# Kernel optimization log

Measured on AMD Instinct MI355X. Metric: run time of the kernel, lower is better.

Reference implementation:

```python
import jax, jax.numpy as jnp
import numpy as np

C = 256          # hidden_size
H = 8            # num_heads
HD = C // H      # head dim = 32
W = 8            # window side; N = W*W = 64 tokens per window
N = W * W
NW = 64          # windows per image
B = 32           # images
B_ = B * NW      # 2048


def make_rel_index():
    # identical to the torch buffer construction (meshgrid 'ij')
    coords = np.stack(np.meshgrid(np.arange(W), np.arange(W), indexing='ij'))  # (2,W,W)
    flat = coords.reshape(2, -1)                       # (2, N)
    rel = flat[:, :, None] - flat[:, None, :]          # (2, N, N)
    rel = rel.transpose(1, 2, 0).astype(np.int64)      # (N, N, 2)
    rel[..., 0] += W - 1
    rel[..., 1] += W - 1
    rel[..., 0] *= 2 * W - 1
    return jnp.asarray(rel.sum(-1), jnp.int32)         # (N, N) in [0, 225)


def setup_inputs() -> dict:
    key = jax.random.key(0)
    ks = jax.random.split(key, 12)
    x = jax.random.normal(ks[0], (B_, N, C), jnp.float32)
    # Swin-style additive mask: 0 for allowed, -1e9 for masked pairs
    keep = jax.random.uniform(ks[1], (NW, N, N)) > 0.1
    mask = jnp.where(keep, 0.0, -1e9).astype(jnp.float32)
    std = 0.02
    wq = jax.random.normal(ks[2], (C, C), jnp.float32) * std
    bq = jnp.zeros((C,), jnp.float32)
    wk = jax.random.normal(ks[3], (C, C), jnp.float32) * std
    bk = jnp.zeros((C,), jnp.float32)
    wv = jax.random.normal(ks[4], (C, C), jnp.float32) * std
    bv = jnp.zeros((C,), jnp.float32)
    wp = jax.random.normal(ks[5], (C, C), jnp.float32) * std
    bp = jnp.zeros((C,), jnp.float32)
    bias_table = jax.random.normal(ks[6], ((2 * W - 1) ** 2, H), jnp.float32) * std
    rel_index = make_rel_index()
    return {"x": x, "mask": mask, "wq": wq, "bq": bq, "wk": wk, "bk": bk,
            "wv": wv, "bv": bv, "wp": wp, "bp": bp,
            "bias_table": bias_table, "rel_index": rel_index}


def reference(x, mask, wq, bq, wk, bk, wv, bv, wp, bp, bias_table, rel_index):
    B_, N, C = x.shape
    nW = mask.shape[0]
    H = bias_table.shape[1]
    HD = C // H
    scale = HD ** -0.5

    def heads(t):  # (B_, N, C) -> (B_, H, N, HD)
        return t.reshape(B_, N, H, HD).transpose(0, 2, 1, 3)

    q = heads(x @ wq + bq) * scale
    k = heads(x @ wk + bk)
    v = heads(x @ wv + bv)

    attn = jnp.einsum('bhnd,bhmd->bhnm', q, k)            # (B_, H, N, N)
    bias = bias_table[rel_index]                          # (N, N, H)
    attn = attn + bias.transpose(2, 0, 1)[None]           # + (1, H, N, N)
    # add per-window shift mask, broadcast over batch and heads
    attn = attn.reshape(B_ // nW, nW, H, N, N) + mask[None, :, None]
    attn = jax.nn.softmax(attn.reshape(B_, H, N, N), axis=-1)

    out = jnp.einsum('bhnm,bhmd->bhnd', attn, v)          # (B_, H, N, HD)
    out = out.transpose(0, 2, 1, 3).reshape(B_, N, C)
    return out @ wp + bp
```

## Files before the change

### kernel.cpp

```cpp
#include <hip/hip_runtime.h>
#include <hip/hip_bf16.h>

typedef __bf16 bf16;
typedef __bf16 bf16x4 __attribute__((ext_vector_type(4)));
typedef __bf16 bf16x8 __attribute__((ext_vector_type(8)));
typedef float  f32x4  __attribute__((ext_vector_type(4)));
typedef short  s16x4  __attribute__((ext_vector_type(4)));

#define DEVI __device__ __forceinline__

static constexpr float kScale = 0.17677669529663687f;

DEVI f32x4 mfma32(bf16x8 a, bf16x8 b, f32x4 c) {
  return __builtin_amdgcn_mfma_f32_16x16x32_bf16(a, b, c, 0, 0, 0);
}
DEVI f32x4 mfma16(bf16x4 a, bf16x4 b, f32x4 c) {
#if __has_builtin(__builtin_amdgcn_mfma_f32_16x16x16bf16_1k)
  return __builtin_amdgcn_mfma_f32_16x16x16bf16_1k(
      __builtin_bit_cast(s16x4, a), __builtin_bit_cast(s16x4, b), c, 0, 0, 0);
#else
  f32x4 d;
  asm volatile("v_mfma_f32_16x16x16_bf16 %0, %1, %2, %3"
               : "=v"(d)
               : "v"(a), "v"(b), "v"(c));
  return d;
#endif
}
DEVI bf16x4 pk4(f32x4 v) {
  bf16x4 p;
  p[0] = (bf16)v[0]; p[1] = (bf16)v[1]; p[2] = (bf16)v[2]; p[3] = (bf16)v[3];
  return p;
}

__global__ __launch_bounds__(256) void prep_kernel(
    const float* __restrict__ wq, const float* __restrict__ bq,
    const float* __restrict__ wk, const float* __restrict__ bk,
    const float* __restrict__ wv, const float* __restrict__ bv,
    const float* __restrict__ wp,
    const float* __restrict__ bias_table, const int* __restrict__ rel_index,
    const float* __restrict__ mask,
    char* __restrict__ wstream, char* __restrict__ wpstream,
    float* __restrict__ bqkv, float* __restrict__ biasM) {
  int idx = blockIdx.x * 256 + threadIdx.x;
  if (idx < 196608) {
    int m = idx >> 16, n = idx & 255, k = (idx >> 8) & 255;
    const float* w = (m == 0) ? wq : (m == 1 ? wk : wv);
    float v = w[k * 256 + n];
    if (m == 0) v *= kScale;
    *(bf16*)(wstream + (size_t)(m * 8 + (k >> 5)) * 16384 + n * 64 +
             (((k & 31) * 2) ^ ((n & 3) << 4))) = (bf16)v;
  } else if (idx < 262144) {
    int rem = idx - 196608;
    int n = rem & 255, k = (rem >> 8) & 255;
    *(bf16*)(wpstream + (size_t)(k >> 5) * 16384 + n * 64 +
             (((k & 31) * 2) ^ ((n & 3) << 4))) = (bf16)wp[k * 256 + n];
  } else if (idx < 262912) {
    int rem = idx - 262144;
    int m = rem >> 8, n = rem & 255;
    const float* b = (m == 0) ? bq : (m == 1 ? bk : bv);
    float v = b[n];
    if (m == 0) v *= kScale;
    bqkv[rem] = v;
  } else if (idx < 2360064) {
    int rem = idx - 262912;
    int w = rem >> 15, h = (rem >> 12) & 7, ij = rem & 4095;
    biasM[rem] = bias_table[rel_index[ij] * 8 + h] + mask[w * 4096 + ij];
  }
}

__global__ __launch_bounds__(256, 2) void swin_kernel(
    const float* __restrict__ x, const char* __restrict__ wstream,
    const char* __restrict__ wpstream, const float* __restrict__ bqkv,
    const float* __restrict__ bp, const float* __restrict__ biasM,
    float* __restrict__ out) {
  __shared__ __align__(16) char xs_ob[32768];
  __shared__ __align__(16) char wbuf[32768];

  int tid = threadIdx.x;
  int w = tid >> 6, lane = tid & 63;
  int g = lane >> 4, c = lane & 15;
  int bid = blockIdx.x;
  int win = (bid & 7) * 256 + ((bid >> 3) & 3) * 64 + (bid >> 5);
  const f32x4 fz = {0.f, 0.f, 0.f, 0.f};

  {
    const char* xw = (const char*)(x + (size_t)win * 16384);
#pragma unroll
    for (int i = 0; i < 8; ++i) {
      int gb = i * 8192 + tid * 32;
      float4 f0 = *(const float4*)(xw + gb);
      float4 f1 = *(const float4*)(xw + gb + 16);
      bf16x8 v;
      v[0] = (bf16)f0.x; v[1] = (bf16)f0.y; v[2] = (bf16)f0.z; v[3] = (bf16)f0.w;
      v[4] = (bf16)f1.x; v[5] = (bf16)f1.y; v[6] = (bf16)f1.z; v[7] = (bf16)f1.w;
      int t = gb >> 10, ir = (gb & 1023) >> 1;
      *(bf16x8*)(xs_ob + ((t * 512 + ir) ^ ((t & 7) << 4))) = v;
    }
  }
  bf16x8 gr[4];
#pragma unroll
  for (int j = 0; j < 4; ++j)
    gr[j] = *(const bf16x8*)(wstream + (size_t)j * 4096 + (size_t)tid * 16);
#pragma unroll
  for (int j = 0; j < 4; ++j)
    *(bf16x8*)(wbuf + j * 4096 + tid * 16) = gr[j];
#pragma unroll
  for (int j = 0; j < 4; ++j)
    gr[j] = *(const bf16x8*)(wstream + 16384 + (size_t)j * 4096 + (size_t)tid * 16);
  __syncthreads();

  bf16x4 qp[4][4], kp[4][4], vp[4][4];
  f32x4 acc[4][4];

  for (int i = 0; i < 24; ++i) {
    int m = i >> 3, kq = i & 7;
    char* cur = wbuf + (i & 1) * 16384;
    char* nxt = wbuf + ((i + 1) & 1) * 16384;

    bf16x8 xf[4], wf[4];
#pragma unroll
    for (int tt = 0; tt < 4; ++tt)
      xf[tt] = *(const bf16x8*)(
          xs_ob + (((tt * 16 + c) * 512 + kq * 64 + g * 16) ^ ((c & 7) << 4)));
#pragma unroll
    for (int nt = 0; nt < 4; ++nt)
      wf[nt] = *(const bf16x8*)(
          cur + (w * 64 + nt * 16 + c) * 64 + ((g * 16) ^ ((c & 3) << 4)));

#pragma unroll
    for (int j = 0; j < 4; ++j)
      *(bf16x8*)(nxt + j * 4096 + tid * 16) = gr[j];
    {
      const char* src = (i < 22) ? (wstream + (size_t)(i + 2) * 16384)
                                 : (wpstream + (size_t)(i - 22) * 16384);
#pragma unroll
      for (int j = 0; j < 4; ++j)
        gr[j] = *(const bf16x8*)(src + (size_t)j * 4096 + (size_t)tid * 16);
    }

    if (kq == 0) {
      if (m < 2) {
#pragma unroll
        for (int nt = 0; nt < 4; ++nt) {
          f32x4 b4 = *(const f32x4*)(bqkv + m * 256 + w * 64 + nt * 16 + g * 4);
#pragma unroll
          for (int tt = 0; tt < 4; ++tt) acc[tt][nt] = b4;
        }
      } else {
#pragma unroll
        for (int nt = 0; nt < 4; ++nt) {
          float bv_ = bqkv[512 + w * 64 + nt * 16 + c];
          f32x4 b4 = {bv_, bv_, bv_, bv_};
#pragma unroll
          for (int tt = 0; tt < 4; ++tt) acc[tt][nt] = b4;
        }
      }
    }
    if (m < 2) {
#pragma unroll
      for (int tt = 0; tt < 4; ++tt)
#pragma unroll
        for (int nt = 0; nt < 4; ++nt)
          acc[tt][nt] = mfma32(wf[nt], xf[tt], acc[tt][nt]);
    } else {
#pragma unroll
      for (int tt = 0; tt < 4; ++tt)
#pragma unroll
        for (int nt = 0; nt < 4; ++nt)
          acc[tt][nt] = mfma32(xf[tt], wf[nt], acc[tt][nt]);
    }
    if (kq == 7) {
#pragma unroll
      for (int tt = 0; tt < 4; ++tt)
#pragma unroll
        for (int nt = 0; nt < 4; ++nt) {
          if (m == 0)      qp[tt][nt] = pk4(acc[tt][nt]);
          else if (m == 1) kp[tt][nt] = pk4(acc[tt][nt]);
          else             vp[tt][nt] = pk4(acc[tt][nt]);
        }
    }
    __syncthreads();
  }

#pragma unroll
  for (int hh = 0; hh < 2; ++hh) {
    int h = w * 2 + hh;
    const float* bm = biasM + ((size_t)(win & 63) * 8 + h) * 4096;
#pragma unroll
    for (int mi = 0; mi < 4; ++mi) {
      f32x4 s[4];
#pragma unroll
      for (int mj = 0; mj < 4; ++mj)
        s[mj] = *(const f32x4*)(bm + (mi * 16 + c) * 64 + mj * 16 + g * 4);
#pragma unroll
      for (int dd = 0; dd < 2; ++dd)
#pragma unroll
        for (int mj = 0; mj < 4; ++mj)
          s[mj] = mfma16(kp[mj][hh * 2 + dd], qp[mi][hh * 2 + dd], s[mj]);
      float mx;
      {
        f32x4 m4 = s[0];
#pragma unroll
        for (int mj = 1; mj < 4; ++mj) {
          m4[0] = fmaxf(m4[0], s[mj][0]); m4[1] = fmaxf(m4[1], s[mj][1]);
          m4[2] = fmaxf(m4[2], s[mj][2]); m4[3] = fmaxf(m4[3], s[mj][3]);
        }
        mx = fmaxf(fmaxf(m4[0], m4[1]), fmaxf(m4[2], m4[3]));
        mx = fmaxf(mx, __shfl_xor(mx, 16));
        mx = fmaxf(mx, __shfl_xor(mx, 32));
      }
      float sum;
      {
        f32x4 s4 = fz;
#pragma unroll
        for (int mj = 0; mj < 4; ++mj) {
#pragma unroll
          for (int r = 0; r < 4; ++r) s[mj][r] = __expf(s[mj][r] - mx);
          s4 += s[mj];
        }
        sum = (s4[0] + s4[1]) + (s4[2] + s4[3]);
        sum += __shfl_xor(sum, 16);
        sum += __shfl_xor(sum, 32);
      }
      float rs = 1.0f / sum;
      bf16x4 pf[4];
#pragma unroll
      for (int mj = 0; mj < 4; ++mj) pf[mj] = pk4(s[mj]);
#pragma unroll
      for (int dt = 0; dt < 2; ++dt) {
        f32x4 o = fz;
#pragma unroll
        for (int mj = 0; mj < 4; ++mj)
          o = mfma16(vp[mj][hh * 2 + dt], pf[mj], o);
        bf16x4 ov;
        ov[0] = (bf16)(o[0] * rs); ov[1] = (bf16)(o[1] * rs);
        ov[2] = (bf16)(o[2] * rs); ov[3] = (bf16)(o[3] * rs);
        *(bf16x4*)(xs_ob + (((mi * 16 + c) * 512 + (h * 32 + dt * 16 + g * 4) * 2) ^
                            ((c & 7) << 4))) = ov;
      }
    }
  }
  __syncthreads();

  f32x4 acc2[4][4];
#pragma unroll
  for (int nt = 0; nt < 4; ++nt) {
    f32x4 b4 = *(const f32x4*)(bp + w * 64 + nt * 16 + g * 4);
#pragma unroll
    for (int tt = 0; tt < 4; ++tt) acc2[tt][nt] = b4;
  }
  for (int i = 24; i < 32; ++i) {
    int cc = i - 24;
    char* cur = wbuf + (i & 1) * 16384;
    char* nxt = wbuf + ((i + 1) & 1) * 16384;

    bf16x8 of[4], wf[4];
#pragma unroll
    for (int tt = 0; tt < 4; ++tt)
      of[tt] = *(const bf16x8*)(
          xs_ob + (((tt * 16 + c) * 512 + cc * 64 + g * 16) ^ ((c & 7) << 4)));
#pragma unroll
    for (int nt = 0; nt < 4; ++nt)
      wf[nt] = *(const bf16x8*)(
          cur + (w * 64 + nt * 16 + c) * 64 + ((g * 16) ^ ((c & 3) << 4)));

    if (i <= 30) {
#pragma unroll
      for (int j = 0; j < 4; ++j)
        *(bf16x8*)(nxt + j * 4096 + tid * 16) = gr[j];
      if (i <= 29) {
#pragma unroll
        for (int j = 0; j < 4; ++j)
          gr[j] = *(const bf16x8*)(wpstream + (size_t)(i - 22) * 16384 +
                                   (size_t)j * 4096 + (size_t)tid * 16);
      }
    }
#pragma unroll
    for (int tt = 0; tt < 4; ++tt)
#pragma unroll
      for (int nt = 0; nt < 4; ++nt)
        acc2[tt][nt] = mfma32(wf[nt], of[tt], acc2[tt][nt]);
    if (i < 31) __syncthreads();
  }
#pragma unroll
  for (int tt = 0; tt < 4; ++tt)
#pragma unroll
    for (int nt = 0; nt < 4; ++nt)
      *(f32x4*)(out + ((size_t)win * 64 + tt * 16 + c) * 256 + w * 64 + nt * 16 + g * 4) =
          acc2[tt][nt];
}

extern "C" void kernel_launch(void* const* d_in, const int* in_sizes, int n_in,
                              void* d_out, int out_size, void* d_ws, size_t ws_size,
                              hipStream_t stream) {
  const float* x          = (const float*)d_in[0];
  const float* mask       = (const float*)d_in[1];
  const float* wq         = (const float*)d_in[2];
  const float* bq         = (const float*)d_in[3];
  const float* wk         = (const float*)d_in[4];
  const float* bk         = (const float*)d_in[5];
  const float* wv         = (const float*)d_in[6];
  const float* bv         = (const float*)d_in[7];
  const float* wp         = (const float*)d_in[8];
  const float* bp         = (const float*)d_in[9];
  const float* bias_table = (const float*)d_in[10];
  const int*   rel_index  = (const int*)d_in[11];

  char* ws = (char*)d_ws;
  size_t o = 0;
  char* wstream = ws + o;  o += (size_t)24 * 16384;
  char* wpstream = ws + o; o += (size_t)8 * 16384;
  float* bqkv = (float*)(ws + o); o += (size_t)768 * 4;
  float* biasM = (float*)(ws + o); o += (size_t)64 * 8 * 64 * 64 * 4;
  if (ws_size < o) return;

  prep_kernel<<<9219, 256, 0, stream>>>(wq, bq, wk, bk, wv, bv, wp,
                                        bias_table, rel_index, mask,
                                        wstream, wpstream, bqkv, biasM);
  swin_kernel<<<2048, 256, 0, stream>>>(x, wstream, wpstream, bqkv, bp, biasM,
                                        (float*)d_out);
}
```

Baseline: 165.5 us.

## Process two windows per 512-thread block sharing weight stream, bf16 bias table

Each block now handles two windows with 512 threads, so every weight chunk staged in shared memory is reused by two windows, halving weight-streaming traffic per window. Weight chunks grow to 64-wide K slices (16 stages instead of 32), which means fewer barriers. The precomputed bias+mask table is stored as bf16, halving its read bandwidth. In exchange the block uses 128KB of LDS with one block per CU, the block-to-window swizzle is dropped, and the bf16 bias costs some precision.

```diff
diff --git a/kernel.cpp b/kernel.cpp
--- a/kernel.cpp
+++ b/kernel.cpp
@@ -39,21 +39,20 @@
     const float* __restrict__ wp,
     const float* __restrict__ bias_table, const int* __restrict__ rel_index,
     const float* __restrict__ mask,
-    char* __restrict__ wstream, char* __restrict__ wpstream,
-    float* __restrict__ bqkv, float* __restrict__ biasM) {
+    char* __restrict__ wsall, float* __restrict__ bqkv, bf16* __restrict__ biasM) {
   int idx = blockIdx.x * 256 + threadIdx.x;
   if (idx < 196608) {
     int m = idx >> 16, n = idx & 255, k = (idx >> 8) & 255;
     const float* w = (m == 0) ? wq : (m == 1 ? wk : wv);
     float v = w[k * 256 + n];
     if (m == 0) v *= kScale;
-    *(bf16*)(wstream + (size_t)(m * 8 + (k >> 5)) * 16384 + n * 64 +
-             (((k & 31) * 2) ^ ((n & 3) << 4))) = (bf16)v;
+    *(bf16*)(wsall + (size_t)(m * 4 + (k >> 6)) * 32768 + n * 128 +
+             (((k & 63) * 2) ^ ((n & 7) << 4))) = (bf16)v;
   } else if (idx < 262144) {
     int rem = idx - 196608;
     int n = rem & 255, k = (rem >> 8) & 255;
-    *(bf16*)(wpstream + (size_t)(k >> 5) * 16384 + n * 64 +
-             (((k & 31) * 2) ^ ((n & 3) << 4))) = (bf16)wp[k * 256 + n];
+    *(bf16*)(wsall + (size_t)(12 + (k >> 6)) * 32768 + n * 128 +
+             (((k & 63) * 2) ^ ((n & 7) << 4))) = (bf16)wp[k * 256 + n];
   } else if (idx < 262912) {
     int rem = idx - 262144;
     int m = rem >> 8, n = rem & 255;
@@ -64,112 +63,105 @@
   } else if (idx < 2360064) {
     int rem = idx - 262912;
     int w = rem >> 15, h = (rem >> 12) & 7, ij = rem & 4095;
-    biasM[rem] = bias_table[rel_index[ij] * 8 + h] + mask[w * 4096 + ij];
-  }
-}
-
-__global__ __launch_bounds__(256, 2) void swin_kernel(
-    const float* __restrict__ x, const char* __restrict__ wstream,
-    const char* __restrict__ wpstream, const float* __restrict__ bqkv,
-    const float* __restrict__ bp, const float* __restrict__ biasM,
-    float* __restrict__ out) {
-  __shared__ __align__(16) char xs_ob[32768];
-  __shared__ __align__(16) char wbuf[32768];
+    biasM[rem] = (bf16)(bias_table[rel_index[ij] * 8 + h] + mask[w * 4096 + ij]);
+  }
+}
+
+__global__ __launch_bounds__(512, 1) void swin_kernel(
+    const float* __restrict__ x, const char* __restrict__ wsall,
+    const float* __restrict__ bqkv, const float* __restrict__ bp,
+    const bf16* __restrict__ biasM, float* __restrict__ out) {
+  __shared__ __align__(16) char xs_ob[65536];
+  __shared__ __align__(16) char wbuf[65536];
 
   int tid = threadIdx.x;
   int w = tid >> 6, lane = tid & 63;
   int g = lane >> 4, c = lane & 15;
-  int bid = blockIdx.x;
-  int win = (bid & 7) * 256 + ((bid >> 3) & 3) * 64 + (bid >> 5);
+  int hw = w >> 2, s = w & 3;
+  int win = blockIdx.x * 2 + hw;
+  char* xs = xs_ob + hw * 32768;
   const f32x4 fz = {0.f, 0.f, 0.f, 0.f};
 
   {
-    const char* xw = (const char*)(x + (size_t)win * 16384);
+    int hw2 = tid >> 8, t256 = tid & 255;
+    const char* xw = (const char*)x + ((size_t)blockIdx.x * 2 + hw2) * 65536;
+    char* xd = xs_ob + hw2 * 32768;
 #pragma unroll
     for (int i = 0; i < 8; ++i) {
-      int gb = i * 8192 + tid * 32;
+      int gb = i * 8192 + t256 * 32;
       float4 f0 = *(const float4*)(xw + gb);
       float4 f1 = *(const float4*)(xw + gb + 16);
       bf16x8 v;
       v[0] = (bf16)f0.x; v[1] = (bf16)f0.y; v[2] = (bf16)f0.z; v[3] = (bf16)f0.w;
       v[4] = (bf16)f1.x; v[5] = (bf16)f1.y; v[6] = (bf16)f1.z; v[7] = (bf16)f1.w;
       int t = gb >> 10, ir = (gb & 1023) >> 1;
-      *(bf16x8*)(xs_ob + ((t * 512 + ir) ^ ((t & 7) << 4))) = v;
+      *(bf16x8*)(xd + ((t * 512 + ir) ^ ((t & 7) << 4))) = v;
     }
   }
   bf16x8 gr[4];
 #pragma unroll
   for (int j = 0; j < 4; ++j)
-    gr[j] = *(const bf16x8*)(wstream + (size_t)j * 4096 + (size_t)tid * 16);
+    gr[j] = *(const bf16x8*)(wsall + (size_t)j * 8192 + (size_t)tid * 16);
 #pragma unroll
   for (int j = 0; j < 4; ++j)
-    *(bf16x8*)(wbuf + j * 4096 + tid * 16) = gr[j];
+    *(bf16x8*)(wbuf + j * 8192 + tid * 16) = gr[j];
 #pragma unroll
   for (int j = 0; j < 4; ++j)
-    gr[j] = *(const bf16x8*)(wstream + 16384 + (size_t)j * 4096 + (size_t)tid * 16);
+    gr[j] = *(const bf16x8*)(wsall + 32768 + (size_t)j * 8192 + (size_t)tid * 16);
   __syncthreads();
 
   bf16x4 qp[4][4], kp[4][4], vp[4][4];
   f32x4 acc[4][4];
 
-  for (int i = 0; i < 24; ++i) {
-    int m = i >> 3, kq = i & 7;
-    char* cur = wbuf + (i & 1) * 16384;
-    char* nxt = wbuf + ((i + 1) & 1) * 16384;
-
-    bf16x8 xf[4], wf[4];
-#pragma unroll
-    for (int tt = 0; tt < 4; ++tt)
-      xf[tt] = *(const bf16x8*)(
-          xs_ob + (((tt * 16 + c) * 512 + kq * 64 + g * 16) ^ ((c & 7) << 4)));
-#pragma unroll
-    for (int nt = 0; nt < 4; ++nt)
-      wf[nt] = *(const bf16x8*)(
-          cur + (w * 64 + nt * 16 + c) * 64 + ((g * 16) ^ ((c & 3) << 4)));
-
-#pragma unroll
-    for (int j = 0; j < 4; ++j)
-      *(bf16x8*)(nxt + j * 4096 + tid * 16) = gr[j];
-    {
-      const char* src = (i < 22) ? (wstream + (size_t)(i + 2) * 16384)
-                                 : (wpstream + (size_t)(i - 22) * 16384);
-#pragma unroll
-      for (int j = 0; j < 4; ++j)
-        gr[j] = *(const bf16x8*)(src + (size_t)j * 4096 + (size_t)tid * 16);
-    }
-
-    if (kq == 0) {
+  for (int i = 0; i < 12; ++i) {
+    int m = i >> 2, kc = i & 3;
+    char* cur = wbuf + (i & 1) * 32768;
+    char* nxt = wbuf + ((i + 1) & 1) * 32768;
+
+    if (kc == 0) {
       if (m < 2) {
 #pragma unroll
         for (int nt = 0; nt < 4; ++nt) {
-          f32x4 b4 = *(const f32x4*)(bqkv + m * 256 + w * 64 + nt * 16 + g * 4);
+          f32x4 b4 = *(const f32x4*)(bqkv + m * 256 + s * 64 + nt * 16 + g * 4);
 #pragma unroll
           for (int tt = 0; tt < 4; ++tt) acc[tt][nt] = b4;
         }
       } else {
 #pragma unroll
         for (int nt = 0; nt < 4; ++nt) {
-          float bv_ = bqkv[512 + w * 64 + nt * 16 + c];
+          float bv_ = bqkv[512 + s * 64 + nt * 16 + c];
           f32x4 b4 = {bv_, bv_, bv_, bv_};
 #pragma unroll
           for (int tt = 0; tt < 4; ++tt) acc[tt][nt] = b4;
         }
       }
     }
-    if (m < 2) {
+#pragma unroll
+    for (int kq2 = 0; kq2 < 2; ++kq2) {
+      bf16x8 xf[4], wf[4];
 #pragma unroll
       for (int tt = 0; tt < 4; ++tt)
-#pragma unroll
-        for (int nt = 0; nt < 4; ++nt)
-          acc[tt][nt] = mfma32(wf[nt], xf[tt], acc[tt][nt]);
-    } else {
-#pragma unroll
-      for (int tt = 0; tt < 4; ++tt)
-#pragma unroll
-        for (int nt = 0; nt < 4; ++nt)
-          acc[tt][nt] = mfma32(xf[tt], wf[nt], acc[tt][nt]);
-    }
-    if (kq == 7) {
+        xf[tt] = *(const bf16x8*)(
+            xs + (((tt * 16 + c) * 512 + kc * 128 + kq2 * 64 + g * 16) ^ ((c & 7) << 4)));
+#pragma unroll
+      for (int nt = 0; nt < 4; ++nt)
+        wf[nt] = *(const bf16x8*)(
+            cur + (s * 64 + nt * 16 + c) * 128 + ((kq2 * 64 + g * 16) ^ ((c & 7) << 4)));
+      if (m < 2) {
+#pragma unroll
+        for (int tt = 0; tt < 4; ++tt)
+#pragma unroll
+          for (int nt = 0; nt < 4; ++nt)
+            acc[tt][nt] = mfma32(wf[nt], xf[tt], acc[tt][nt]);
+      } else {
+#pragma unroll
+        for (int tt = 0; tt < 4; ++tt)
+#pragma unroll
+          for (int nt = 0; nt < 4; ++nt)
+            acc[tt][nt] = mfma32(xf[tt], wf[nt], acc[tt][nt]);
+      }
+    }
+    if (kc == 3) {
 #pragma unroll
       for (int tt = 0; tt < 4; ++tt)
 #pragma unroll
@@ -179,31 +171,42 @@
           else             vp[tt][nt] = pk4(acc[tt][nt]);
         }
     }
+#pragma unroll
+    for (int j = 0; j < 4; ++j)
+      *(bf16x8*)(nxt + j * 8192 + tid * 16) = gr[j];
+    if (i + 2 <= 15) {
+#pragma unroll
+      for (int j = 0; j < 4; ++j)
+        gr[j] = *(const bf16x8*)(wsall + (size_t)(i + 2) * 32768 +
+                                 (size_t)j * 8192 + (size_t)tid * 16);
+    }
     __syncthreads();
   }
 
 #pragma unroll
   for (int hh = 0; hh < 2; ++hh) {
-    int h = w * 2 + hh;
-    const float* bm = biasM + ((size_t)(win & 63) * 8 + h) * 4096;
+    int h = s * 2 + hh;
+    const bf16* bm = biasM + ((size_t)(win & 63) * 8 + h) * 4096;
 #pragma unroll
     for (int mi = 0; mi < 4; ++mi) {
-      f32x4 s[4];
-#pragma unroll
-      for (int mj = 0; mj < 4; ++mj)
-        s[mj] = *(const f32x4*)(bm + (mi * 16 + c) * 64 + mj * 16 + g * 4);
+      f32x4 sv[4];
+#pragma unroll
+      for (int mj = 0; mj < 4; ++mj) {
+        bf16x4 b4 = *(const bf16x4*)(bm + (mi * 16 + c) * 64 + mj * 16 + g * 4);
+        sv[mj] = (f32x4){(float)b4[0], (float)b4[1], (float)b4[2], (float)b4[3]};
+      }
 #pragma unroll
       for (int dd = 0; dd < 2; ++dd)
 #pragma unroll
         for (int mj = 0; mj < 4; ++mj)
-          s[mj] = mfma16(kp[mj][hh * 2 + dd], qp[mi][hh * 2 + dd], s[mj]);
+          sv[mj] = mfma16(kp[mj][hh * 2 + dd], qp[mi][hh * 2 + dd], sv[mj]);
       float mx;
       {
-        f32x4 m4 = s[0];
+        f32x4 m4 = sv[0];
 #pragma unroll
         for (int mj = 1; mj < 4; ++mj) {
-          m4[0] = fmaxf(m4[0], s[mj][0]); m4[1] = fmaxf(m4[1], s[mj][1]);
-          m4[2] = fmaxf(m4[2], s[mj][2]); m4[3] = fmaxf(m4[3], s[mj][3]);
+          m4[0] = fmaxf(m4[0], sv[mj][0]); m4[1] = fmaxf(m4[1], sv[mj][1]);
+          m4[2] = fmaxf(m4[2], sv[mj][2]); m4[3] = fmaxf(m4[3], sv[mj][3]);
         }
         mx = fmaxf(fmaxf(m4[0], m4[1]), fmaxf(m4[2], m4[3]));
         mx = fmaxf(mx, __shfl_xor(mx, 16));
@@ -215,8 +218,8 @@
 #pragma unroll
         for (int mj = 0; mj < 4; ++mj) {
 #pragma unroll
-          for (int r = 0; r < 4; ++r) s[mj][r] = __expf(s[mj][r] - mx);
-          s4 += s[mj];
+          for (int r = 0; r < 4; ++r) sv[mj][r] = __expf(sv[mj][r] - mx);
+          s4 += sv[mj];
         }
         sum = (s4[0] + s4[1]) + (s4[2] + s4[3]);
         sum += __shfl_xor(sum, 16);
@@ -225,7 +228,7 @@
       float rs = 1.0f / sum;
       bf16x4 pf[4];
 #pragma unroll
-      for (int mj = 0; mj < 4; ++mj) pf[mj] = pk4(s[mj]);
+      for (int mj = 0; mj < 4; ++mj) pf[mj] = pk4(sv[mj]);
 #pragma unroll
       for (int dt = 0; dt < 2; ++dt) {
         f32x4 o = fz;
@@ -235,8 +238,8 @@
         bf16x4 ov;
         ov[0] = (bf16)(o[0] * rs); ov[1] = (bf16)(o[1] * rs);
         ov[2] = (bf16)(o[2] * rs); ov[3] = (bf16)(o[3] * rs);
-        *(bf16x4*)(xs_ob + (((mi * 16 + c) * 512 + (h * 32 + dt * 16 + g * 4) * 2) ^
-                            ((c & 7) << 4))) = ov;
+        *(bf16x4*)(xs + (((mi * 16 + c) * 512 + (h * 32 + dt * 16 + g * 4) * 2) ^
+                         ((c & 7) << 4))) = ov;
       }
     }
   }
@@ -245,48 +248,49 @@
   f32x4 acc2[4][4];
 #pragma unroll
   for (int nt = 0; nt < 4; ++nt) {
-    f32x4 b4 = *(const f32x4*)(bp + w * 64 + nt * 16 + g * 4);
+    f32x4 b4 = *(const f32x4*)(bp + s * 64 + nt * 16 + g * 4);
 #pragma unroll
     for (int tt = 0; tt < 4; ++tt) acc2[tt][nt] = b4;
   }
-  for (int i = 24; i < 32; ++i) {
-    int cc = i - 24;
-    char* cur = wbuf + (i & 1) * 16384;
-    char* nxt = wbuf + ((i + 1) & 1) * 16384;
-
-    bf16x8 of[4], wf[4];
-#pragma unroll
-    for (int tt = 0; tt < 4; ++tt)
-      of[tt] = *(const bf16x8*)(
-          xs_ob + (((tt * 16 + c) * 512 + cc * 64 + g * 16) ^ ((c & 7) << 4)));
+  for (int i = 12; i < 16; ++i) {
+    int kc = i - 12;
+    char* cur = wbuf + (i & 1) * 32768;
+    char* nxt = wbuf + ((i + 1) & 1) * 32768;
+#pragma unroll
+    for (int kq2 = 0; kq2 < 2; ++kq2) {
+      bf16x8 of[4], wf[4];
+#pragma unroll
+      for (int tt = 0; tt < 4; ++tt)
+        of[tt] = *(const bf16x8*)(
+            xs + (((tt * 16 + c) * 512 + kc * 128 + kq2 * 64 + g * 16) ^ ((c & 7) << 4)));
+#pragma unroll
+      for (int nt = 0; nt < 4; ++nt)
+        wf[nt] = *(const bf16x8*)(
+            cur + (s * 64 + nt * 16 + c) * 128 + ((kq2 * 64 + g * 16) ^ ((c & 7) << 4)));
+#pragma unroll
+      for (int tt = 0; tt < 4; ++tt)
+#pragma unroll
+        for (int nt = 0; nt < 4; ++nt)
+          acc2[tt][nt] = mfma32(wf[nt], of[tt], acc2[tt][nt]);
+    }
+    if (i < 15) {
+#pragma unroll
+      for (int j = 0; j < 4; ++j)
+        *(bf16x8*)(nxt + j * 8192 + tid * 16) = gr[j];
+      if (i + 2 <= 15) {
+#pragma unroll
+        for (int j = 0; j < 4; ++j)
+          gr[j] = *(const bf16x8*)(wsall + (size_t)(i + 2) * 32768 +
+                                   (size_t)j * 8192 + (size_t)tid * 16);
+      }
+      __syncthreads();
+    }
+  }
+#pragma unroll
+  for (int tt = 0; tt < 4; ++tt)
 #pragma unroll
     for (int nt = 0; nt < 4; ++nt)
-      wf[nt] = *(const bf16x8*)(
-          cur + (w * 64 + nt * 16 + c) * 64 + ((g * 16) ^ ((c & 3) << 4)));
-
-    if (i <= 30) {
-#pragma unroll
-      for (int j = 0; j < 4; ++j)
-        *(bf16x8*)(nxt + j * 4096 + tid * 16) = gr[j];
-      if (i <= 29) {
-#pragma unroll
-        for (int j = 0; j < 4; ++j)
-          gr[j] = *(const bf16x8*)(wpstream + (size_t)(i - 22) * 16384 +
-                                   (size_t)j * 4096 + (size_t)tid * 16);
-      }
-    }
-#pragma unroll
-    for (int tt = 0; tt < 4; ++tt)
-#pragma unroll
-      for (int nt = 0; nt < 4; ++nt)
-        acc2[tt][nt] = mfma32(wf[nt], of[tt], acc2[tt][nt]);
-    if (i < 31) __syncthreads();
-  }
-#pragma unroll
-  for (int tt = 0; tt < 4; ++tt)
-#pragma unroll
-    for (int nt = 0; nt < 4; ++nt)
-      *(f32x4*)(out + ((size_t)win * 64 + tt * 16 + c) * 256 + w * 64 + nt * 16 + g * 4) =
+      *(f32x4*)(out + ((size_t)win * 64 + tt * 16 + c) * 256 + s * 64 + nt * 16 + g * 4) =
           acc2[tt][nt];
 }
 
@@ -308,15 +312,13 @@
 
   char* ws = (char*)d_ws;
   size_t o = 0;
-  char* wstream = ws + o;  o += (size_t)24 * 16384;
-  char* wpstream = ws + o; o += (size_t)8 * 16384;
+  char* wsall = ws + o; o += (size_t)16 * 32768;
   float* bqkv = (float*)(ws + o); o += (size_t)768 * 4;
-  float* biasM = (float*)(ws + o); o += (size_t)64 * 8 * 64 * 64 * 4;
+  bf16* biasM = (bf16*)(ws + o); o += (size_t)64 * 8 * 64 * 64 * 2;
   if (ws_size < o) return;
 
   prep_kernel<<<9219, 256, 0, stream>>>(wq, bq, wk, bk, wv, bv, wp,
                                         bias_table, rel_index, mask,
-                                        wstream, wpstream, bqkv, biasM);
-  swin_kernel<<<2048, 256, 0, stream>>>(x, wstream, wpstream, bqkv, bp, biasM,
-                                        (float*)d_out);
-}
+                                        wsall, bqkv, biasM);
+  swin_kernel<<<1024, 512, 0, stream>>>(x, wsall, bqkv, bp, biasM, (float*)d_out);
+}
```

New measurement: 155.7 us, median of 2. -5.9%, faster.
